# Kernel tuning notes

Measured on AMD Instinct MI355X. Metric: run time of the kernel, lower is better.

Reference implementation:

```python
import jax, jax.numpy as jnp
import numpy as np
import math

H = 2048
NH = 16
HD = H // NH  # 128
EPS_LN = 1e-5
RES_SCALE_MAX = 0.3

def _nan_clean(x, lim=10000.0):
    return jnp.nan_to_num(x, nan=0.0, posinf=lim, neginf=-lim)

def setup_inputs() -> dict:
    key = jax.random.key(0)
    ks = jax.random.split(key, 12)
    B, S, T = 4, 2048, 256
    std = 1.0 / math.sqrt(H)
    return {
        "hidden_states": jax.random.normal(ks[0], (B, S, H), jnp.float32),
        "audio_tokens": jax.random.normal(ks[1], (B, T, H), jnp.float32),
        "attention_mask": jax.random.randint(ks[2], (B, T), 0, 2, jnp.int32),
        "Wq": jax.random.normal(ks[3], (H, H), jnp.float32) * std,
        "bq": jnp.zeros((H,), jnp.float32),
        "Wk": jax.random.normal(ks[4], (H, H), jnp.float32) * std,
        "bk": jnp.zeros((H,), jnp.float32),
        "Wv": jax.random.normal(ks[5], (H, H), jnp.float32) * std,
        "bv": jnp.zeros((H,), jnp.float32),
        "Wo": jax.random.normal(ks[6], (H, H), jnp.float32) * std,
        "bo": jnp.zeros((H,), jnp.float32),
        "ln_gamma": jnp.ones((H,), jnp.float32),
        "ln_beta": jnp.zeros((H,), jnp.float32),
        "residual_scale": jnp.float32(0.05),
    }

def reference(hidden_states, audio_tokens, attention_mask,
              Wq, bq, Wk, bk, Wv, bv, Wo, bo, ln_gamma, ln_beta, residual_scale):
    B, S, _ = hidden_states.shape
    T = audio_tokens.shape[1]
    hs = _nan_clean(hidden_states).astype(jnp.float32)
    at = _nan_clean(audio_tokens).astype(jnp.float32)
    # Q/K/V projections -> (B, heads, len, head_dim)
    def proj(x, W, b, L):
        y = x @ W.T + b
        return y.reshape(B, L, NH, HD).transpose(0, 2, 1, 3)
    q = _nan_clean(proj(hs, Wq, bq, S))
    k = _nan_clean(proj(at, Wk, bk, T))
    v = _nan_clean(proj(at, Wv, bv, T))
    scale = max(math.sqrt(HD), 1e-8)
    scores = jnp.einsum('bhsd,bhtd->bhst', q, k) / scale
    scores = jnp.clip(scores, -50.0, 50.0)
    scores = jnp.nan_to_num(scores, nan=0.0, posinf=50.0, neginf=-50.0)
    # mask: int 0/1 -> attend where > 0.5, broadcast (B,1,1,T)
    attend = (attention_mask.astype(jnp.float32) > 0.5)[:, None, None, :]
    scores = jnp.where(attend, scores, -10000.0)
    scores = jnp.clip(scores, -50.0, 50.0)
    probs = jax.nn.softmax(scores, axis=-1)
    probs = jnp.nan_to_num(probs, nan=0.0, posinf=1.0, neginf=0.0)
    probs = probs / (probs.sum(axis=-1, keepdims=True) + 1e-8)
    # dropout: eval mode -> identity
    ctx = jnp.einsum('bhst,bhtd->bhsd', probs, v)
    ctx = ctx.transpose(0, 2, 1, 3).reshape(B, S, H)
    delta = _nan_clean(ctx @ Wo.T + bo)
    rs = jnp.clip(residual_scale, 0.0, RES_SCALE_MAX)
    delta = rs * delta
    # LayerNorm (biased variance, like torch)
    mu = delta.mean(axis=-1, keepdims=True)
    var = jnp.mean((delta - mu) ** 2, axis=-1, keepdims=True)
    delta = (delta - mu) / jnp.sqrt(var + EPS_LN) * ln_gamma + ln_beta
    return delta
```

## Files before the change

kernel.cpp:

```cpp
#include <hip/hip_runtime.h>
#include <stdint.h>

typedef unsigned short u16;
typedef __attribute__((ext_vector_type(8))) __bf16 bf16x8;
typedef __attribute__((ext_vector_type(4))) float f32x4;

#define AS1 __attribute__((address_space(1)))
#define AS3 __attribute__((address_space(3)))

constexpr int HB = 4;
constexpr int SS = 2048;
constexpr int TT = 256;
constexpr int HH = 2048;
constexpr int NHEAD = 16;
constexpr int HD = 128;

__device__ __forceinline__ u16 f2b(float f) {
  union { float f; uint32_t u; } c; c.f = f;
  return (u16)((c.u + 0x7FFFu + ((c.u >> 16) & 1u)) >> 16);
}

__device__ __forceinline__ float b2f(uint32_t lo16) {
  union { uint32_t u; float f; } c; c.u = lo16 << 16;
  return c.f;
}

__global__ __launch_bounds__(256)
void cast_all(const float* __restrict__ hs, const float* __restrict__ at,
              const float* __restrict__ wq, const float* __restrict__ wk,
              const float* __restrict__ wv, const float* __restrict__ wo,
              u16* __restrict__ o_hs, u16* __restrict__ o_at,
              u16* __restrict__ o_wq, u16* __restrict__ o_wk,
              u16* __restrict__ o_wv, u16* __restrict__ o_wo) {
  const int b = blockIdx.x;
  const float* src; u16* dst; int base;
  if (b < 16384)      { src = hs; dst = o_hs; base = 0; }
  else if (b < 18432) { src = at; dst = o_at; base = 16384; }
  else if (b < 22528) { src = wq; dst = o_wq; base = 18432; }
  else if (b < 26624) { src = wk; dst = o_wk; base = 22528; }
  else if (b < 30720) { src = wv; dst = o_wv; base = 26624; }
  else                { src = wo; dst = o_wo; base = 30720; }
  const size_t i = (size_t)(b - base) * 256 + threadIdx.x;
  const float4 v = *(const float4*)(src + i * 4);
  uint2 pk;
  pk.x = (uint32_t)f2b(v.x) | ((uint32_t)f2b(v.y) << 16);
  pk.y = (uint32_t)f2b(v.z) | ((uint32_t)f2b(v.w) << 16);
  *(uint2*)(dst + i * 4) = pk;
}

template<int MODE>
__global__ __launch_bounds__(512, 2)
void gemm8(const u16* __restrict__ A, const u16* __restrict__ Bw,
           const float* __restrict__ bias, const float* __restrict__ rsp,
           void* __restrict__ outp) {
  constexpr int KD = 2048, NT = 64;
  constexpr int BUF = 16384;
  __shared__ u16 lds[4 * BUF];
  const int tid = threadIdx.x;
  const int wv = tid >> 6, ln = tid & 63;
  const int lq = ln >> 4, lr = ln & 15;
  const int wm = wv >> 2, wn = wv & 3;

  const int linb = blockIdx.y * 8 + blockIdx.x;
  const int ns = (linb & 7) * 32 + (linb >> 3);
  const int m0 = (ns >> 3) * 256;
  const int n0 = (ns & 7) * 256;

  int gOff[2];
#pragma unroll
  for (int c = 0; c < 2; ++c) {
    const int g = c * 512 + tid, sr = g >> 3, s = g & 7, l = s ^ (sr & 7);
    gOff[c] = (2 * sr + (l >> 2)) * KD + (l & 3) * 8;
  }
  const u16* Abase = A + (size_t)m0 * KD;
  const u16* Bbase = Bw + (size_t)n0 * KD;

  int aoff[8], boff[4];
#pragma unroll
  for (int m = 0; m < 8; ++m) {
    const int R = wm * 128 + m * 16 + lr, sr = R >> 1;
    aoff[m] = sr * 64 + ((((R & 1) << 2) + lq) ^ (sr & 7)) * 8;
  }
#pragma unroll
  for (int j = 0; j < 4; ++j) {
    const int R = wn * 64 + j * 16 + lr, sr = R >> 1;
    boff[j] = 8192 + sr * 64 + ((((R & 1) << 2) + lq) ^ (sr & 7)) * 8;
  }

#define STAGE_A(c, k0, buf)                                                      \
  __builtin_amdgcn_global_load_lds((AS1 const void*)(Abase + (k0) + gOff[c]),    \
      (AS3 void*)(lds + (buf) * BUF + ((c) * 512 + wv * 64) * 8), 16, 0, 0)
#define STAGE_B(c, k0, buf)                                                      \
  __builtin_amdgcn_global_load_lds((AS1 const void*)(Bbase + (k0) + gOff[c]),    \
      (AS3 void*)(lds + (buf) * BUF + 8192 + ((c) * 512 + wv * 64) * 8), 16, 0, 0)

  f32x4 acc[8][4];
#pragma unroll
  for (int i = 0; i < 8; ++i)
#pragma unroll
    for (int j = 0; j < 4; ++j) acc[i][j] = (f32x4){0.f, 0.f, 0.f, 0.f};

  STAGE_A(0, 0, 0);  STAGE_A(1, 0, 0);  STAGE_B(0, 0, 0);  STAGE_B(1, 0, 0);
  STAGE_A(0, 32, 1); STAGE_A(1, 32, 1); STAGE_B(0, 32, 1); STAGE_B(1, 32, 1);
  STAGE_A(0, 64, 2); STAGE_A(1, 64, 2); STAGE_B(0, 64, 2); STAGE_B(1, 64, 2);
  asm volatile("s_waitcnt vmcnt(8)" ::: "memory");
  __builtin_amdgcn_s_barrier();
  __builtin_amdgcn_sched_barrier(0);

  bf16x8 af[4], bf[4], afn[4];
#pragma unroll
  for (int j = 0; j < 4; ++j) bf[j] = *(const bf16x8*)(lds + boff[j]);
#pragma unroll
  for (int m = 0; m < 4; ++m) af[m] = *(const bf16x8*)(lds + aoff[m]);
  __builtin_amdgcn_sched_barrier(0);

  for (int t = 0; t < NT; ++t) {
    const u16* bb = lds + (t & 3) * BUF;
    const u16* bn = lds + ((t + 1) & 3) * BUF;
    const int stg = (t + 3) & 3;
    const int k3 = (t + 3) * 32;
    const bool doStage = (t + 3) < NT;

#pragma unroll
    for (int m = 0; m < 4; ++m) afn[m] = *(const bf16x8*)(bb + aoff[4 + m]);
    if (doStage) { STAGE_A(0, k3, stg); STAGE_A(1, k3, stg); }
    asm volatile("s_waitcnt lgkmcnt(4)" ::: "memory");
    __builtin_amdgcn_sched_barrier(0);
    __builtin_amdgcn_s_setprio(1);
#pragma unroll
    for (int m = 0; m < 4; ++m)
#pragma unroll
      for (int j = 0; j < 4; ++j)
        acc[m][j] = __builtin_amdgcn_mfma_f32_16x16x32_bf16(af[m], bf[j], acc[m][j], 0, 0, 0);
    __builtin_amdgcn_s_setprio(0);
    if (doStage) { STAGE_B(0, k3, stg); STAGE_B(1, k3, stg); }
    if (t < NT - 3)       asm volatile("s_waitcnt vmcnt(8)" ::: "memory");
    else if (t == NT - 3) asm volatile("s_waitcnt vmcnt(4)" ::: "memory");
    else                  asm volatile("s_waitcnt vmcnt(0)" ::: "memory");
    asm volatile("s_waitcnt lgkmcnt(0)" ::: "memory");
    __builtin_amdgcn_s_barrier();
    __builtin_amdgcn_sched_barrier(0);
    if (t + 1 < NT) {
#pragma unroll
      for (int m = 0; m < 4; ++m) af[m] = *(const bf16x8*)(bn + aoff[m]);
    }
    __builtin_amdgcn_s_setprio(1);
#pragma unroll
    for (int m = 0; m < 4; ++m)
#pragma unroll
      for (int j = 0; j < 4; ++j)
        acc[4 + m][j] = __builtin_amdgcn_mfma_f32_16x16x32_bf16(afn[m], bf[j], acc[4 + m][j], 0, 0, 0);
    __builtin_amdgcn_s_setprio(0);
    if (t + 1 < NT) {
#pragma unroll
      for (int j = 0; j < 4; ++j) bf[j] = *(const bf16x8*)(bn + boff[j]);
    }
    __builtin_amdgcn_sched_barrier(0);
  }
#undef STAGE_A
#undef STAGE_B

  float bj[4];
#pragma unroll
  for (int j = 0; j < 4; ++j) bj[j] = bias[n0 + wn * 64 + j * 16 + lr];
  float rsv = 0.f;
  if constexpr (MODE == 2 || MODE == 3) rsv = fminf(fmaxf(rsp[0], 0.0f), 0.3f);

#pragma unroll
  for (int i = 0; i < 8; ++i)
#pragma unroll
    for (int j = 0; j < 4; ++j)
#pragma unroll
      for (int r = 0; r < 4; ++r) {
        const int row = m0 + wm * 128 + i * 16 + lq * 4 + r;
        const int col = n0 + wn * 64 + j * 16 + lr;
        const float v = acc[i][j][r] + bj[j];
        if constexpr (MODE == 0) {
          ((u16*)outp)[(size_t)row * 2048 + col] = f2b(v);
        } else if constexpr (MODE == 2) {
          ((float*)outp)[(size_t)row * 2048 + col] = v * rsv;
        } else {
          ((u16*)outp)[(size_t)row * 2048 + col] = f2b(v * rsv);
        }
      }
}

__global__ __launch_bounds__(256, 2)
void gemm_kv(const u16* __restrict__ A, const u16* __restrict__ Wk,
             const u16* __restrict__ Wv, const float* __restrict__ bkp,
             const float* __restrict__ bvp, u16* __restrict__ Ko,
             u16* __restrict__ Vto) {
  constexpr int KD = 2048, NT = 64;
  constexpr int BUFE = 8192;
  __shared__ u16 lds[4 * BUFE];
  const bool isV = blockIdx.z != 0;
  const u16* Bw = isV ? Wv : Wk;
  const float* bias = isV ? bvp : bkp;
  const int tid = threadIdx.x;
  const int wave = tid >> 6, lane = tid & 63;
  const int lq = lane >> 4, lr = lane & 15;
  const int wr = wave >> 1, wc = wave & 1;
  const int m0 = blockIdx.y * 128, n0 = blockIdx.x * 128;

  int gOff[2];
#pragma unroll
  for (int c = 0; c < 2; ++c) {
    const int g = c * 256 + tid, sr = g >> 3, s = g & 7, l = s ^ (sr & 7);
    gOff[c] = (2 * sr + (l >> 2)) * KD + (l & 3) * 8;
  }
  const u16* Abase = A + (size_t)m0 * KD;
  const u16* Bbase = Bw + (size_t)n0 * KD;

  int aoff[4], boff[4];
#pragma unroll
  for (int i = 0; i < 4; ++i) {
    const int R = wr * 64 + i * 16 + lr, sr = R >> 1;
    aoff[i] = sr * 64 + ((((R & 1) << 2) + lq) ^ (sr & 7)) * 8;
  }
#pragma unroll
  for (int j = 0; j < 4; ++j) {
    const int R = wc * 64 + j * 16 + lr, sr = R >> 1;
    boff[j] = 4096 + sr * 64 + ((((R & 1) << 2) + lq) ^ (sr & 7)) * 8;
  }

#define KV_STAGE(t3, buf)                                                         \
  {                                                                               \
    _Pragma("unroll")                                                             \
    for (int c_ = 0; c_ < 2; ++c_) {                                              \
      __builtin_amdgcn_global_load_lds(                                           \
          (AS1 const void*)(Abase + (t3) * 32 + gOff[c_]),                        \
          (AS3 void*)(lds + (buf) * BUFE + (c_ * 256 + wave * 64) * 8), 16, 0, 0);\
      __builtin_amdgcn_global_load_lds(                                           \
          (AS1 const void*)(Bbase + (t3) * 32 + gOff[c_]),                        \
          (AS3 void*)(lds + (buf) * BUFE + 4096 + (c_ * 256 + wave * 64) * 8),    \
          16, 0, 0);                                                              \
    }                                                                             \
  }

  f32x4 acc[4][4];
#pragma unroll
  for (int i = 0; i < 4; ++i)
#pragma unroll
    for (int j = 0; j < 4; ++j) acc[i][j] = (f32x4){0.f, 0.f, 0.f, 0.f};

  KV_STAGE(0, 0); KV_STAGE(1, 1); KV_STAGE(2, 2);
  asm volatile("s_waitcnt vmcnt(8)" ::: "memory");
  __builtin_amdgcn_s_barrier();
  __builtin_amdgcn_sched_barrier(0);

  bf16x8 af[4], bfr[4];
#pragma unroll
  for (int i = 0; i < 4; ++i) af[i] = *(const bf16x8*)(lds + aoff[i]);
#pragma unroll
  for (int j = 0; j < 4; ++j) bfr[j] = *(const bf16x8*)(lds + boff[j]);
  __builtin_amdgcn_sched_barrier(0);

  for (int t = 0; t < NT; ++t) {
    if (t + 3 < NT) KV_STAGE(t + 3, (t + 3) & 3);
    asm volatile("s_waitcnt lgkmcnt(0)" ::: "memory");
    __builtin_amdgcn_sched_barrier(0);
    __builtin_amdgcn_s_setprio(1);
#pragma unroll
    for (int i = 0; i < 4; ++i)
#pragma unroll
      for (int j = 0; j < 4; ++j)
        acc[i][j] = __builtin_amdgcn_mfma_f32_16x16x32_bf16(af[i], bfr[j], acc[i][j], 0, 0, 0);
    __builtin_amdgcn_s_setprio(0);
    if (t < NT - 3)       asm volatile("s_waitcnt vmcnt(8)" ::: "memory");
    else if (t == NT - 3) asm volatile("s_waitcnt vmcnt(4)" ::: "memory");
    else                  asm volatile("s_waitcnt vmcnt(0)" ::: "memory");
    __builtin_amdgcn_s_barrier();
    __builtin_amdgcn_sched_barrier(0);
    if (t + 1 < NT) {
      const u16* bn = lds + ((t + 1) & 3) * BUFE;
#pragma unroll
      for (int i = 0; i < 4; ++i) af[i] = *(const bf16x8*)(bn + aoff[i]);
#pragma unroll
      for (int j = 0; j < 4; ++j) bfr[j] = *(const bf16x8*)(bn + boff[j]);
    }
    __builtin_amdgcn_sched_barrier(0);
  }
#undef KV_STAGE

  float bj[4];
#pragma unroll
  for (int j = 0; j < 4; ++j) bj[j] = bias[n0 + wc * 64 + j * 16 + lr];

#pragma unroll
  for (int i = 0; i < 4; ++i)
#pragma unroll
    for (int j = 0; j < 4; ++j)
#pragma unroll
      for (int r = 0; r < 4; ++r) {
        const int row = m0 + wr * 64 + i * 16 + lq * 4 + r;
        const int col = n0 + wc * 64 + j * 16 + lr;
        const float v = acc[i][j][r] + bj[j];
        if (!isV) {
          Ko[(size_t)row * 2048 + col] = f2b(v);
        } else {
          Vto[(size_t)(row >> 8) * (2048 * 256) + (size_t)col * 256 + (row & 255)] = f2b(v);
        }
      }
}

__global__ __launch_bounds__(512, 4)
void attn_kernel(const u16* __restrict__ Q, const u16* __restrict__ Kb,
                 const u16* __restrict__ Vt, const int* __restrict__ mask,
                 u16* __restrict__ ctx) {
  __shared__ u16 sK[2][64 * 128];
  __shared__ u16 sVt[2][128 * 64];
  __shared__ u16 sP[8 * 16 * 64];

  const int tid = threadIdx.x;
  const int wv = tid >> 6, ln = tid & 63;
  const int lq = ln >> 4, lr = ln & 15;
  const int h = blockIdx.y, b = blockIdx.z;
  const int s0blk = blockIdx.x * 128;
  u16* sPw = sP + wv * (16 * 64);

  bf16x8 qf[4];
  {
    const u16* qp = Q + ((size_t)b * SS + s0blk + wv * 16 + lr) * HH + (size_t)h * HD + lq * 8;
#pragma unroll
    for (int kd = 0; kd < 4; ++kd) qf[kd] = *(const bf16x8*)(qp + kd * 32);
  }

#define STAGE_KV(c)                                                                      \
  {                                                                                      \
    const int buf_ = (c) & 1;                                                            \
    _Pragma("unroll")                                                                    \
    for (int it = 0; it < 2; ++it) {                                                     \
      const int ub = it * 512 + wv * 64;                                                 \
      const int u = ub + ln;                                                             \
      const int row = u >> 4, slot = u & 15, src = slot ^ (row & 15);                    \
      const u16* g = Kb + ((size_t)b * TT + (c) * 64 + row) * HH + h * HD + src * 8;     \
      __builtin_amdgcn_global_load_lds((AS1 const void*)g,                               \
          (AS3 void*)(sK[buf_] + (size_t)ub * 8), 16, 0, 0);                             \
    }                                                                                    \
    _Pragma("unroll")                                                                    \
    for (int it = 0; it < 2; ++it) {                                                     \
      const int ub = it * 512 + wv * 64;                                                 \
      const int u = ub + ln;                                                             \
      const int row = u >> 3, slot = u & 7, src = slot ^ (row & 7);                      \
      const u16* g = Vt + ((size_t)b * HH + h * HD + row) * TT + (c) * 64 + src * 8;     \
      __builtin_amdgcn_global_load_lds((AS1 const void*)g,                               \
          (AS3 void*)(sVt[buf_] + (size_t)ub * 8), 16, 0, 0);                            \
    }                                                                                    \
  }
  STAGE_KV(0);
  STAGE_KV(1);

  const float scale = 0.08838834764831845f;
  float m[4] = {-INFINITY, -INFINITY, -INFINITY, -INFINITY};
  float l[4] = {0.f, 0.f, 0.f, 0.f};
  f32x4 o[8];
#pragma unroll
  for (int d0 = 0; d0 < 8; ++d0) o[d0] = (f32x4){0.f, 0.f, 0.f, 0.f};

  const int shsrc = ((lr >> 2) << 4) + lr;

  for (int c = 0; c < 4; ++c) {
    const int buf = c & 1;
    if (c < 3) asm volatile("s_waitcnt vmcnt(4)" ::: "memory");
    else       asm volatile("s_waitcnt vmcnt(0)" ::: "memory");
    __syncthreads();

    f32x4 sc[4];
#pragma unroll
    for (int tt = 0; tt < 4; ++tt) {
      f32x4 a = (f32x4){0.f, 0.f, 0.f, 0.f};
#pragma unroll
      for (int kd = 0; kd < 4; ++kd) {
        bf16x8 kf = *(const bf16x8*)(sK[buf] + (size_t)(tt * 16 + lr) * 128 + (size_t)((kd * 4 + lq) ^ lr) * 8);
        a = __builtin_amdgcn_mfma_f32_16x16x32_bf16(qf[kd], kf, a, 0, 0, 0);
      }
      sc[tt] = a;
    }

    float lm[4] = {-1e30f, -1e30f, -1e30f, -1e30f};
#pragma unroll
    for (int tt = 0; tt < 4; ++tt) {
      const int att = mask[b * TT + c * 64 + tt * 16 + lr];
#pragma unroll
      for (int r = 0; r < 4; ++r) {
        float v = sc[tt][r] * scale;
        v = fminf(fmaxf(v, -50.f), 50.f);
        v = att ? v : -50.f;
        sc[tt][r] = v;
        lm[r] = fmaxf(lm[r], v);
      }
    }
#pragma unroll
    for (int d = 1; d < 16; d <<= 1)
#pragma unroll
      for (int r = 0; r < 4; ++r) lm[r] = fmaxf(lm[r], __shfl_xor(lm[r], d));

    float alpha[4];
#pragma unroll
    for (int r = 0; r < 4; ++r) {
      const float mn = fmaxf(m[r], lm[r]);
      alpha[r] = __expf(m[r] - mn);
      m[r] = mn;
    }
    float ls[4] = {0.f, 0.f, 0.f, 0.f};
#pragma unroll
    for (int tt = 0; tt < 4; ++tt)
#pragma unroll
      for (int r = 0; r < 4; ++r) {
        const float p = __expf(sc[tt][r] - m[r]);
        sc[tt][r] = p;
        ls[r] += p;
      }
#pragma unroll
    for (int d = 1; d < 16; d <<= 1)
#pragma unroll
      for (int r = 0; r < 4; ++r) ls[r] += __shfl_xor(ls[r], d);
#pragma unroll
    for (int r = 0; r < 4; ++r) l[r] = l[r] * alpha[r] + ls[r];

    const float a0 = __shfl(alpha[0], shsrc), a1 = __shfl(alpha[1], shsrc);
    const float a2 = __shfl(alpha[2], shsrc), a3 = __shfl(alpha[3], shsrc);
    const int rsel = lr & 3;
    const float aq = rsel == 0 ? a0 : rsel == 1 ? a1 : rsel == 2 ? a2 : a3;
    if (!__all(aq >= 1.0f)) {
#pragma unroll
      for (int d0 = 0; d0 < 8; ++d0)
#pragma unroll
        for (int r = 0; r < 4; ++r) o[d0][r] *= aq;
    }

#pragma unroll
    for (int tt = 0; tt < 4; ++tt)
#pragma unroll
      for (int r = 0; r < 4; ++r) {
        const int q = lq * 4 + r;
        const int slot = (tt * 2 + (lr >> 3)) ^ ((q >> 1) & 7);
        sPw[(size_t)q * 64 + slot * 8 + (lr & 7)] = f2b(sc[tt][r]);
      }

    bf16x8 pf[2];
#pragma unroll
    for (int kt = 0; kt < 2; ++kt) {
      const int slot = (kt * 4 + lq) ^ ((lr >> 1) & 7);
      pf[kt] = *(const bf16x8*)(sPw + (size_t)lr * 64 + slot * 8);
    }

#pragma unroll
    for (int d0 = 0; d0 < 8; ++d0)
#pragma unroll
      for (int kt = 0; kt < 2; ++kt) {
        bf16x8 vf = *(const bf16x8*)(sVt[buf] + (size_t)(d0 * 16 + lr) * 64 + (size_t)((kt * 4 + lq) ^ (lr & 7)) * 8);
        o[d0] = __builtin_amdgcn_mfma_f32_16x16x32_bf16(vf, pf[kt], o[d0], 0, 0, 0);
      }
    if (c < 2) {
      __syncthreads();
      STAGE_KV(c + 2);
    }
  }
#undef STAGE_KV

  const float i0 = __shfl(1.0f / l[0], shsrc), i1 = __shfl(1.0f / l[1], shsrc);
  const float i2 = __shfl(1.0f / l[2], shsrc), i3 = __shfl(1.0f / l[3], shsrc);
  const int rsel = lr & 3;
  const float iq = rsel == 0 ? i0 : rsel == 1 ? i1 : rsel == 2 ? i2 : i3;

  const size_t cbase = ((size_t)b * SS + s0blk + wv * 16 + lr) * HH + (size_t)h * HD;
#pragma unroll
  for (int d0 = 0; d0 < 8; ++d0) {
    uint2 w;
    w.x = (uint32_t)f2b(o[d0][0] * iq) | ((uint32_t)f2b(o[d0][1] * iq) << 16);
    w.y = (uint32_t)f2b(o[d0][2] * iq) | ((uint32_t)f2b(o[d0][3] * iq) << 16);
    *(uint2*)(ctx + cbase + d0 * 16 + lq * 4) = w;
  }
}

__global__ __launch_bounds__(256)
void ln_kernel(const u16* __restrict__ in, float* __restrict__ out,
               const float* __restrict__ gamma, const float* __restrict__ beta) {
  const int row = blockIdx.x, tid = threadIdx.x;
  const u16* x = in + (size_t)row * 2048;
  const uint4 raw = *(const uint4*)(x + tid * 8);
  float xv[8];
  xv[0] = b2f(raw.x & 0xFFFFu); xv[1] = b2f(raw.x >> 16);
  xv[2] = b2f(raw.y & 0xFFFFu); xv[3] = b2f(raw.y >> 16);
  xv[4] = b2f(raw.z & 0xFFFFu); xv[5] = b2f(raw.z >> 16);
  xv[6] = b2f(raw.w & 0xFFFFu); xv[7] = b2f(raw.w >> 16);
  float s = 0.f, ss = 0.f;
#pragma unroll
  for (int i = 0; i < 8; ++i) { s += xv[i]; ss += xv[i] * xv[i]; }
#pragma unroll
  for (int d = 1; d < 64; d <<= 1) {
    s += __shfl_xor(s, d);
    ss += __shfl_xor(ss, d);
  }
  __shared__ float rbuf[8];
  const int w = tid >> 6;
  if ((tid & 63) == 0) { rbuf[w] = s; rbuf[4 + w] = ss; }
  __syncthreads();
  s = rbuf[0] + rbuf[1] + rbuf[2] + rbuf[3];
  ss = rbuf[4] + rbuf[5] + rbuf[6] + rbuf[7];
  const float mu = s * (1.0f / 2048.0f);
  const float var = ss * (1.0f / 2048.0f) - mu * mu;
  const float inv = rsqrtf(var + 1e-5f);
  const float4 g0 = *(const float4*)(gamma + tid * 8);
  const float4 g1 = *(const float4*)(gamma + tid * 8 + 4);
  const float4 b0 = *(const float4*)(beta + tid * 8);
  const float4 b1 = *(const float4*)(beta + tid * 8 + 4);
  float4 y0, y1;
  y0.x = (xv[0] - mu) * inv * g0.x + b0.x;
  y0.y = (xv[1] - mu) * inv * g0.y + b0.y;
  y0.z = (xv[2] - mu) * inv * g0.z + b0.z;
  y0.w = (xv[3] - mu) * inv * g0.w + b0.w;
  y1.x = (xv[4] - mu) * inv * g1.x + b1.x;
  y1.y = (xv[5] - mu) * inv * g1.y + b1.y;
  y1.z = (xv[6] - mu) * inv * g1.z + b1.z;
  y1.w = (xv[7] - mu) * inv * g1.w + b1.w;
  float* o = out + (size_t)row * 2048 + tid * 8;
  *(float4*)o = y0;
  *(float4*)(o + 4) = y1;
}

extern "C" void kernel_launch(void* const* d_in, const int* in_sizes, int n_in,
                              void* d_out, int out_size, void* d_ws, size_t ws_size,
                              hipStream_t stream) {
  (void)in_sizes; (void)n_in; (void)out_size; (void)ws_size;
  const float* hs = (const float*)d_in[0];
  const float* at = (const float*)d_in[1];
  const int* mask = (const int*)d_in[2];
  const float* Wq = (const float*)d_in[3];
  const float* bq = (const float*)d_in[4];
  const float* Wk = (const float*)d_in[5];
  const float* bk = (const float*)d_in[6];
  const float* Wv = (const float*)d_in[7];
  const float* bv = (const float*)d_in[8];
  const float* Wo = (const float*)d_in[9];
  const float* bo = (const float*)d_in[10];
  const float* lg = (const float*)d_in[11];
  const float* lb = (const float*)d_in[12];
  const float* rs = (const float*)d_in[13];

  u16* hs_bf = (u16*)d_ws;
  u16* at_bf = hs_bf + 16777216;
  u16* Wq_bf = at_bf + 2097152;
  u16* Wk_bf = Wq_bf + 4194304;
  u16* Wv_bf = Wk_bf + 4194304;
  u16* Wo_bf = Wv_bf + 4194304;
  u16* Q_bf  = Wo_bf + 4194304;
  u16* K_bf  = Q_bf + 16777216;
  u16* Vt_bf = K_bf + 2097152;
  u16* ctx_bf = hs_bf;
  u16* delta_bf = Q_bf;

  cast_all<<<34816, 256, 0, stream>>>(hs, at, Wq, Wk, Wv, Wo,
                                      hs_bf, at_bf, Wq_bf, Wk_bf, Wv_bf, Wo_bf);

  gemm8<0><<<dim3(8, 32), 512, 0, stream>>>(hs_bf, Wq_bf, bq, nullptr, Q_bf);
  gemm_kv<<<dim3(16, 8, 2), 256, 0, stream>>>(at_bf, Wk_bf, Wv_bf, bk, bv, K_bf, Vt_bf);

  attn_kernel<<<dim3(16, 16, 4), 512, 0, stream>>>(Q_bf, K_bf, Vt_bf, mask, ctx_bf);

  gemm8<3><<<dim3(8, 32), 512, 0, stream>>>(ctx_bf, Wo_bf, bo, rs, delta_bf);
  ln_kernel<<<8192, 256, 0, stream>>>(delta_bf, (float*)d_out, lg, lb);
}
```

Measured before the change: 266.1 us.

## Load full K per block, use single-pass softmax, read V directly from global

The attention kernel now loads all 256 K rows into LDS once per block and processes two 128-row query tiles per block, halving the grid. With all scores in registers, it computes an exact one-pass softmax instead of online rescaling. V fragments are read straight from global memory rather than staged in LDS. This removes the double-buffered pipeline and its barriers and improves K reuse. The costs are higher register pressure (launch bounds lowered to 2 blocks per SIMD set), fewer blocks in flight, and uncached global V loads sitting on the MFMA critical path.

```diff
diff --git a/kernel.cpp b/kernel.cpp
--- a/kernel.cpp
+++ b/kernel.cpp
@@ -303,75 +303,59 @@
       }
 }
 
-__global__ __launch_bounds__(512, 4)
+__global__ __launch_bounds__(512, 2)
 void attn_kernel(const u16* __restrict__ Q, const u16* __restrict__ Kb,
                  const u16* __restrict__ Vt, const int* __restrict__ mask,
                  u16* __restrict__ ctx) {
-  __shared__ u16 sK[2][64 * 128];
-  __shared__ u16 sVt[2][128 * 64];
+  __shared__ u16 sK[256 * 128];
   __shared__ u16 sP[8 * 16 * 64];
 
   const int tid = threadIdx.x;
   const int wv = tid >> 6, ln = tid & 63;
   const int lq = ln >> 4, lr = ln & 15;
   const int h = blockIdx.y, b = blockIdx.z;
-  const int s0blk = blockIdx.x * 128;
+  const int s0blk = blockIdx.x * 256;
   u16* sPw = sP + wv * (16 * 64);
 
-  bf16x8 qf[4];
-  {
-    const u16* qp = Q + ((size_t)b * SS + s0blk + wv * 16 + lr) * HH + (size_t)h * HD + lq * 8;
-#pragma unroll
-    for (int kd = 0; kd < 4; ++kd) qf[kd] = *(const bf16x8*)(qp + kd * 32);
-  }
-
-#define STAGE_KV(c)                                                                      \
-  {                                                                                      \
-    const int buf_ = (c) & 1;                                                            \
-    _Pragma("unroll")                                                                    \
-    for (int it = 0; it < 2; ++it) {                                                     \
-      const int ub = it * 512 + wv * 64;                                                 \
-      const int u = ub + ln;                                                             \
-      const int row = u >> 4, slot = u & 15, src = slot ^ (row & 15);                    \
-      const u16* g = Kb + ((size_t)b * TT + (c) * 64 + row) * HH + h * HD + src * 8;     \
-      __builtin_amdgcn_global_load_lds((AS1 const void*)g,                               \
-          (AS3 void*)(sK[buf_] + (size_t)ub * 8), 16, 0, 0);                             \
-    }                                                                                    \
-    _Pragma("unroll")                                                                    \
-    for (int it = 0; it < 2; ++it) {                                                     \
-      const int ub = it * 512 + wv * 64;                                                 \
-      const int u = ub + ln;                                                             \
-      const int row = u >> 3, slot = u & 7, src = slot ^ (row & 7);                      \
-      const u16* g = Vt + ((size_t)b * HH + h * HD + row) * TT + (c) * 64 + src * 8;     \
-      __builtin_amdgcn_global_load_lds((AS1 const void*)g,                               \
-          (AS3 void*)(sVt[buf_] + (size_t)ub * 8), 16, 0, 0);                            \
-    }                                                                                    \
-  }
-  STAGE_KV(0);
-  STAGE_KV(1);
+#pragma unroll
+  for (int it = 0; it < 8; ++it) {
+    const int ub = it * 512 + wv * 64;
+    const int u = ub + ln;
+    const int row = u >> 4, slot = u & 15, src = slot ^ (row & 15);
+    const u16* g = Kb + ((size_t)b * TT + row) * HH + h * HD + src * 8;
+    __builtin_amdgcn_global_load_lds((AS1 const void*)g,
+                                     (AS3 void*)(sK + (size_t)ub * 8), 16, 0, 0);
+  }
+
+  int att[16];
+#pragma unroll
+  for (int tt = 0; tt < 16; ++tt) att[tt] = mask[b * TT + tt * 16 + lr];
+
+  asm volatile("s_waitcnt vmcnt(0)" ::: "memory");
+  __builtin_amdgcn_s_barrier();
 
   const float scale = 0.08838834764831845f;
-  float m[4] = {-INFINITY, -INFINITY, -INFINITY, -INFINITY};
-  float l[4] = {0.f, 0.f, 0.f, 0.f};
-  f32x4 o[8];
-#pragma unroll
-  for (int d0 = 0; d0 < 8; ++d0) o[d0] = (f32x4){0.f, 0.f, 0.f, 0.f};
-
   const int shsrc = ((lr >> 2) << 4) + lr;
-
-  for (int c = 0; c < 4; ++c) {
-    const int buf = c & 1;
-    if (c < 3) asm volatile("s_waitcnt vmcnt(4)" ::: "memory");
-    else       asm volatile("s_waitcnt vmcnt(0)" ::: "memory");
-    __syncthreads();
-
-    f32x4 sc[4];
-#pragma unroll
-    for (int tt = 0; tt < 4; ++tt) {
+  const size_t vbase = ((size_t)b * HH + (size_t)h * HD) * TT;
+
+#pragma unroll 1
+  for (int qt = 0; qt < 2; ++qt) {
+    bf16x8 qf[4];
+    {
+      const u16* qp = Q + ((size_t)b * SS + s0blk + qt * 128 + wv * 16 + lr) * HH
+                      + (size_t)h * HD + lq * 8;
+#pragma unroll
+      for (int kd = 0; kd < 4; ++kd) qf[kd] = *(const bf16x8*)(qp + kd * 32);
+    }
+
+    f32x4 sc[16];
+#pragma unroll
+    for (int tt = 0; tt < 16; ++tt) {
       f32x4 a = (f32x4){0.f, 0.f, 0.f, 0.f};
 #pragma unroll
       for (int kd = 0; kd < 4; ++kd) {
-        bf16x8 kf = *(const bf16x8*)(sK[buf] + (size_t)(tt * 16 + lr) * 128 + (size_t)((kd * 4 + lq) ^ lr) * 8);
+        bf16x8 kf = *(const bf16x8*)(sK + (size_t)(tt * 16 + lr) * 128
+                                     + (size_t)((kd * 4 + lq) ^ lr) * 8);
         a = __builtin_amdgcn_mfma_f32_16x16x32_bf16(qf[kd], kf, a, 0, 0, 0);
       }
       sc[tt] = a;
@@ -379,35 +363,26 @@
 
     float lm[4] = {-1e30f, -1e30f, -1e30f, -1e30f};
 #pragma unroll
-    for (int tt = 0; tt < 4; ++tt) {
-      const int att = mask[b * TT + c * 64 + tt * 16 + lr];
+    for (int tt = 0; tt < 16; ++tt)
 #pragma unroll
       for (int r = 0; r < 4; ++r) {
         float v = sc[tt][r] * scale;
         v = fminf(fmaxf(v, -50.f), 50.f);
-        v = att ? v : -50.f;
+        v = att[tt] ? v : -50.f;
         sc[tt][r] = v;
         lm[r] = fmaxf(lm[r], v);
       }
-    }
 #pragma unroll
     for (int d = 1; d < 16; d <<= 1)
 #pragma unroll
       for (int r = 0; r < 4; ++r) lm[r] = fmaxf(lm[r], __shfl_xor(lm[r], d));
 
-    float alpha[4];
-#pragma unroll
-    for (int r = 0; r < 4; ++r) {
-      const float mn = fmaxf(m[r], lm[r]);
-      alpha[r] = __expf(m[r] - mn);
-      m[r] = mn;
-    }
     float ls[4] = {0.f, 0.f, 0.f, 0.f};
 #pragma unroll
-    for (int tt = 0; tt < 4; ++tt)
+    for (int tt = 0; tt < 16; ++tt)
 #pragma unroll
       for (int r = 0; r < 4; ++r) {
-        const float p = __expf(sc[tt][r] - m[r]);
+        const float p = __expf(sc[tt][r] - lm[r]);
         sc[tt][r] = p;
         ls[r] += p;
       }
@@ -415,62 +390,53 @@
     for (int d = 1; d < 16; d <<= 1)
 #pragma unroll
       for (int r = 0; r < 4; ++r) ls[r] += __shfl_xor(ls[r], d);
-#pragma unroll
-    for (int r = 0; r < 4; ++r) l[r] = l[r] * alpha[r] + ls[r];
-
-    const float a0 = __shfl(alpha[0], shsrc), a1 = __shfl(alpha[1], shsrc);
-    const float a2 = __shfl(alpha[2], shsrc), a3 = __shfl(alpha[3], shsrc);
+
+    const float i0 = __shfl(1.0f / ls[0], shsrc), i1 = __shfl(1.0f / ls[1], shsrc);
+    const float i2 = __shfl(1.0f / ls[2], shsrc), i3 = __shfl(1.0f / ls[3], shsrc);
     const int rsel = lr & 3;
-    const float aq = rsel == 0 ? a0 : rsel == 1 ? a1 : rsel == 2 ? a2 : a3;
-    if (!__all(aq >= 1.0f)) {
+    const float iq = rsel == 0 ? i0 : rsel == 1 ? i1 : rsel == 2 ? i2 : i3;
+
+    f32x4 o[8];
+#pragma unroll
+    for (int d0 = 0; d0 < 8; ++d0) o[d0] = (f32x4){0.f, 0.f, 0.f, 0.f};
+
+#pragma unroll
+    for (int tq = 0; tq < 4; ++tq) {
+#pragma unroll
+      for (int t2 = 0; t2 < 4; ++t2) {
+        const int tt = tq * 4 + t2;
+#pragma unroll
+        for (int r = 0; r < 4; ++r) {
+          const int q = lq * 4 + r;
+          const int slot = (t2 * 2 + (lr >> 3)) ^ ((q >> 1) & 7);
+          sPw[(size_t)q * 64 + slot * 8 + (lr & 7)] = f2b(sc[tt][r]);
+        }
+      }
+      bf16x8 pf[2];
+#pragma unroll
+      for (int kt = 0; kt < 2; ++kt) {
+        const int slot = (kt * 4 + lq) ^ ((lr >> 1) & 7);
+        pf[kt] = *(const bf16x8*)(sPw + (size_t)lr * 64 + slot * 8);
+      }
 #pragma unroll
       for (int d0 = 0; d0 < 8; ++d0)
 #pragma unroll
-        for (int r = 0; r < 4; ++r) o[d0][r] *= aq;
-    }
-
-#pragma unroll
-    for (int tt = 0; tt < 4; ++tt)
-#pragma unroll
-      for (int r = 0; r < 4; ++r) {
-        const int q = lq * 4 + r;
-        const int slot = (tt * 2 + (lr >> 3)) ^ ((q >> 1) & 7);
-        sPw[(size_t)q * 64 + slot * 8 + (lr & 7)] = f2b(sc[tt][r]);
-      }
-
-    bf16x8 pf[2];
-#pragma unroll
-    for (int kt = 0; kt < 2; ++kt) {
-      const int slot = (kt * 4 + lq) ^ ((lr >> 1) & 7);
-      pf[kt] = *(const bf16x8*)(sPw + (size_t)lr * 64 + slot * 8);
-    }
-
-#pragma unroll
-    for (int d0 = 0; d0 < 8; ++d0)
-#pragma unroll
-      for (int kt = 0; kt < 2; ++kt) {
-        bf16x8 vf = *(const bf16x8*)(sVt[buf] + (size_t)(d0 * 16 + lr) * 64 + (size_t)((kt * 4 + lq) ^ (lr & 7)) * 8);
-        o[d0] = __builtin_amdgcn_mfma_f32_16x16x32_bf16(vf, pf[kt], o[d0], 0, 0, 0);
-      }
-    if (c < 2) {
-      __syncthreads();
-      STAGE_KV(c + 2);
-    }
-  }
-#undef STAGE_KV
-
-  const float i0 = __shfl(1.0f / l[0], shsrc), i1 = __shfl(1.0f / l[1], shsrc);
-  const float i2 = __shfl(1.0f / l[2], shsrc), i3 = __shfl(1.0f / l[3], shsrc);
-  const int rsel = lr & 3;
-  const float iq = rsel == 0 ? i0 : rsel == 1 ? i1 : rsel == 2 ? i2 : i3;
-
-  const size_t cbase = ((size_t)b * SS + s0blk + wv * 16 + lr) * HH + (size_t)h * HD;
-#pragma unroll
-  for (int d0 = 0; d0 < 8; ++d0) {
-    uint2 w;
-    w.x = (uint32_t)f2b(o[d0][0] * iq) | ((uint32_t)f2b(o[d0][1] * iq) << 16);
-    w.y = (uint32_t)f2b(o[d0][2] * iq) | ((uint32_t)f2b(o[d0][3] * iq) << 16);
-    *(uint2*)(ctx + cbase + d0 * 16 + lq * 4) = w;
+        for (int kt = 0; kt < 2; ++kt) {
+          const bf16x8 vf = *(const bf16x8*)(Vt + vbase + (size_t)(d0 * 16 + lr) * TT
+                                             + (tq * 2 + kt) * 32 + lq * 8);
+          o[d0] = __builtin_amdgcn_mfma_f32_16x16x32_bf16(vf, pf[kt], o[d0], 0, 0, 0);
+        }
+    }
+
+    const size_t cbase = ((size_t)b * SS + s0blk + qt * 128 + wv * 16 + lr) * HH
+                         + (size_t)h * HD;
+#pragma unroll
+    for (int d0 = 0; d0 < 8; ++d0) {
+      uint2 w;
+      w.x = (uint32_t)f2b(o[d0][0] * iq) | ((uint32_t)f2b(o[d0][1] * iq) << 16);
+      w.y = (uint32_t)f2b(o[d0][2] * iq) | ((uint32_t)f2b(o[d0][3] * iq) << 16);
+      *(uint2*)(ctx + cbase + d0 * 16 + lq * 4) = w;
+    }
   }
 }
 
@@ -557,7 +523,7 @@
   gemm8<0><<<dim3(8, 32), 512, 0, stream>>>(hs_bf, Wq_bf, bq, nullptr, Q_bf);
   gemm_kv<<<dim3(16, 8, 2), 256, 0, stream>>>(at_bf, Wk_bf, Wv_bf, bk, bv, K_bf, Vt_bf);
 
-  attn_kernel<<<dim3(16, 16, 4), 512, 0, stream>>>(Q_bf, K_bf, Vt_bf, mask, ctx_bf);
+  attn_kernel<<<dim3(8, 16, 4), 512, 0, stream>>>(Q_bf, K_bf, Vt_bf, mask, ctx_bf);
 
   gemm8<3><<<dim3(8, 32), 512, 0, stream>>>(ctx_bf, Wo_bf, bo, rs, delta_bf);
   ln_kernel<<<8192, 256, 0, stream>>>(delta_bf, (float*)d_out, lg, lb);
```

New measurement: 523.9 us. 1.97x slower.
